# Kernel optimization log

Measured on AMD Instinct MI355X. Metric: run time of the kernel, lower is better.

The kernel has to match this reference:

```python
import jax, jax.numpy as jnp
import numpy as np

HEAD_SIZE = 64


def setup_inputs() -> dict:
    key = jax.random.key(0)
    ks = jax.random.split(key, 6)
    B, S, D, H = 8, 2048, 1024, HEAD_SIZE
    return {
        "q": jax.random.normal(ks[0], (B, S, D), dtype=jnp.float32),
        "k": jax.random.normal(ks[1], (B, S, D), dtype=jnp.float32),
        "v": jax.random.normal(ks[2], (B, S, D), dtype=jnp.float32),
        "mask": jnp.ones((B, S), dtype=bool),
        "Wq": jax.random.normal(ks[3], (D, H), dtype=jnp.float32) * (D ** -0.5),
        "Wk": jax.random.normal(ks[4], (D, H), dtype=jnp.float32) * (D ** -0.5),
        "Wv": jax.random.normal(ks[5], (D, H), dtype=jnp.float32) * (D ** -0.5),
    }


def reference(q, k, v, mask, Wq, Wk, Wv):
    # Linear projections (bias=False): x @ W, W is [n_embd, head_size]
    qp = jnp.einsum("bsd,dh->bsh", q, Wq)
    kp = jnp.einsum("bsd,dh->bsh", k, Wk)
    vp = jnp.einsum("bsd,dh->bsh", v, Wv)
    scale = HEAD_SIZE ** -0.5
    scores = jnp.einsum("bqh,bkh->bqk", qp, kp) * scale  # [B, Sq, Sk]
    # 2-D mask [B, Sk] -> broadcast over query dim (mask.unsqueeze(1))
    scores = jnp.where(mask[:, None, :], scores, -jnp.inf)
    attn = jax.nn.softmax(scores, axis=-1)
    # dropout is identity in eval mode (deterministic reference)
    out = jnp.einsum("bqk,bkh->bqh", attn, vp)
    return out
```

## Files before the change

### kernel.cpp

```cpp
#include <hip/hip_runtime.h>
#include <hip/hip_bf16.h>
#include <math.h>

#define B_ 8
#define S_ 2048
#define D_ 1024
#define H_ 64
#define M_ (B_*S_)
#define SPLIT 4
#define KPS (S_/SPLIT)

typedef __attribute__((ext_vector_type(8))) short bf16x8;
typedef __attribute__((ext_vector_type(8))) unsigned short u16x8;
typedef __attribute__((ext_vector_type(4))) float f32x4;

__device__ inline unsigned short f2bf(float f) {
    unsigned int u = __builtin_bit_cast(unsigned int, f);
    u += 0x7fffu + ((u >> 16) & 1u);
    return (unsigned short)(u >> 16);
}

__device__ inline void async16(const void* g, void* l) {
    __builtin_amdgcn_global_load_lds((const __attribute__((address_space(1))) void*)g,
                                     (__attribute__((address_space(3))) void*)l, 16, 0, 0);
}

__global__ __launch_bounds__(256) void mask_kernel(const unsigned char* __restrict__ mask,
                                                   float* __restrict__ mmul, int n) {
    int j = blockIdx.x * 256 + threadIdx.x;
    if (j >= n) return;
    bool boolLayout = mask[1] != 0;
    int mv = boolLayout ? (int)mask[j] : ((const int*)mask)[j];
    mmul[j] = mv ? 1.0f : 0.0f;
}

__global__ __launch_bounds__(256) void wprep_kernel(
    const float* __restrict__ Wq, const float* __restrict__ Wk, const float* __restrict__ Wv,
    unsigned short* __restrict__ Wt)
{
    const int m = blockIdx.y;
    const float* W = (m == 0) ? Wq : (m == 1) ? Wk : Wv;
    unsigned short* Wo = Wt + (size_t)m * 64 * 1024;
    __shared__ unsigned short T[64][65];
    const int t = threadIdx.x;
    const int k0 = blockIdx.x * 64;
    #pragma unroll
    for (int i = 0; i < 16; i++) {
        int vi = t + i * 256;
        int kk = vi >> 6, n = vi & 63;
        T[kk][n] = f2bf(W[(size_t)(k0 + kk) * 64 + n]);
    }
    __syncthreads();
    #pragma unroll
    for (int i = 0; i < 4; i++) {
        int vi = t + i * 256;
        int n = vi >> 4, k4 = vi & 15;
        ushort4 u;
        u.x = T[k4*4+0][n]; u.y = T[k4*4+1][n]; u.z = T[k4*4+2][n]; u.w = T[k4*4+3][n];
        *(ushort4*)&Wo[(size_t)n * 1024 + k0 + k4*4] = u;
    }
}

__global__ __launch_bounds__(256) void proj_kernel(
    const float* __restrict__ q, const float* __restrict__ kx, const float* __restrict__ vx,
    const unsigned short* __restrict__ Wt,
    unsigned short* __restrict__ qp, unsigned short* __restrict__ kp, unsigned short* __restrict__ vpT)
{
    const int m = blockIdx.y;
    const float* x = (m == 0) ? q : (m == 1) ? kx : vx;
    const unsigned short* Wm = Wt + (size_t)m * 64 * 1024;

    const int t = threadIdx.x;
    const int w = t >> 6, l = t & 63;
    const int lrow = l & 15, quad = l >> 4;
    const int row0 = blockIdx.x * 64;

    const float* xa = x + (size_t)(row0 + w * 16 + lrow) * D_ + quad * 8;
    const unsigned short* wb = Wm + (size_t)lrow * D_ + quad * 8;

    f32x4 acc[4] = {};

    #pragma unroll 2
    for (int k = 0; k < D_; k += 32) {
        f32x4 a0 = *(const f32x4*)(xa + k);
        f32x4 a1 = *(const f32x4*)(xa + k + 4);
        bf16x8 b0 = *(const bf16x8*)(wb + k);
        bf16x8 b1 = *(const bf16x8*)(wb + 16 * D_ + k);
        bf16x8 b2 = *(const bf16x8*)(wb + 32 * D_ + k);
        bf16x8 b3 = *(const bf16x8*)(wb + 48 * D_ + k);
        bf16x8 af;
        af[0] = (short)f2bf(a0.x); af[1] = (short)f2bf(a0.y);
        af[2] = (short)f2bf(a0.z); af[3] = (short)f2bf(a0.w);
        af[4] = (short)f2bf(a1.x); af[5] = (short)f2bf(a1.y);
        af[6] = (short)f2bf(a1.z); af[7] = (short)f2bf(a1.w);
        acc[0] = __builtin_amdgcn_mfma_f32_16x16x32_bf16(af, b0, acc[0], 0, 0, 0);
        acc[1] = __builtin_amdgcn_mfma_f32_16x16x32_bf16(af, b1, acc[1], 0, 0, 0);
        acc[2] = __builtin_amdgcn_mfma_f32_16x16x32_bf16(af, b2, acc[2], 0, 0, 0);
        acc[3] = __builtin_amdgcn_mfma_f32_16x16x32_bf16(af, b3, acc[3], 0, 0, 0);
    }

    const int orow = row0 + w * 16 + quad * 4;
    if (m < 2) {
        unsigned short* outp = (m == 0) ? qp : kp;
        const float sc = (m == 0) ? 0.125f : 1.0f;
        #pragma unroll
        for (int c = 0; c < 4; c++)
            #pragma unroll
            for (int rr = 0; rr < 4; rr++)
                outp[(size_t)(orow + rr) * H_ + c * 16 + lrow] = f2bf(acc[c][rr] * sc);
    } else {
        const int bb = orow >> 11;
        const int s0 = orow & (S_ - 1);
        #pragma unroll
        for (int c = 0; c < 4; c++) {
            ushort4 u;
            u.x = f2bf(acc[c][0]); u.y = f2bf(acc[c][1]);
            u.z = f2bf(acc[c][2]); u.w = f2bf(acc[c][3]);
            *(ushort4*)&vpT[((size_t)bb * H_ + c * 16 + lrow) * S_ + s0] = u;
        }
    }
}

__global__ __launch_bounds__(256) void attn_kernel(
    const unsigned short* __restrict__ qp, const unsigned short* __restrict__ kp,
    const unsigned short* __restrict__ vpT, const float* __restrict__ mmul,
    float* __restrict__ po, float* __restrict__ pl)
{
    __shared__ unsigned short Qs[64][72];
    __shared__ unsigned short Ps[64][72];
    __shared__ unsigned short Ks[64 * 64];
    __shared__ unsigned short Vt[64 * 64];

    const int t = threadIdx.x;
    const int w = t >> 6, l = t & 63;
    const int lrow = l & 15, quad = l >> 4;
    const int b = blockIdx.y, q0 = blockIdx.x * 64, split = blockIdx.z;
    const int key0 = split * KPS;
    const size_t basebs = (size_t)b * S_;
    const unsigned short* vb = vpT + (size_t)b * H_ * S_;

    #pragma unroll
    for (int i = 0; i < 2; i++) {
        int p = t + i * 256;
        int r = p >> 3, c8 = p & 7;
        u16x8 u = *(const u16x8*)&qp[(basebs + q0 + r) * H_ + c8 * 8];
        *(u16x8*)&Qs[r][c8 * 8] = u;
    }

    float lsum[4] = {0.f, 0.f, 0.f, 0.f};
    f32x4 o[4] = {};

    for (int kt = 0; kt < KPS / 64; kt++) {
        const int k0 = key0 + kt * 64;
        __syncthreads();
        #pragma unroll
        for (int j = 0; j < 2; j++) {
            int p = (w * 2 + j) * 64 + l;
            int r = p >> 3;
            int c8 = (p & 7) ^ (r & 7);
            async16(&kp[(basebs + k0 + r) * H_ + c8 * 8], &Ks[p * 8]);
        }
        #pragma unroll
        for (int j = 0; j < 2; j++) {
            int p = (w * 2 + j) * 64 + l;
            int h = p >> 3;
            int c8 = (p & 7) ^ (h & 7);
            async16(&vb[(size_t)h * S_ + k0 + c8 * 8], &Vt[p * 8]);
        }
        float mm[4];
        #pragma unroll
        for (int c = 0; c < 4; c++) mm[c] = mmul[basebs + k0 + c*16 + lrow];
        __syncthreads();

        f32x4 s[4] = {};
        #pragma unroll
        for (int kk = 0; kk < 2; kk++) {
            bf16x8 aq = *(const bf16x8*)&Qs[w*16 + lrow][kk*32 + quad*8];
            #pragma unroll
            for (int c = 0; c < 4; c++) {
                const int n = c*16 + lrow;
                bf16x8 bk = *(const bf16x8*)&Ks[(n * 8 + ((kk*4 + quad) ^ (n & 7))) * 8];
                s[c] = __builtin_amdgcn_mfma_f32_16x16x32_bf16(aq, bk, s[c], 0, 0, 0);
            }
        }
        #pragma unroll
        for (int r = 0; r < 4; r++) {
            float p0 = __expf(s[0][r]) * mm[0];
            float p1 = __expf(s[1][r]) * mm[1];
            float p2 = __expf(s[2][r]) * mm[2];
            float p3 = __expf(s[3][r]) * mm[3];
            lsum[r] += (p0 + p1) + (p2 + p3);
            const int pr = w*16 + quad*4 + r;
            Ps[pr][ 0 + lrow] = f2bf(p0);
            Ps[pr][16 + lrow] = f2bf(p1);
            Ps[pr][32 + lrow] = f2bf(p2);
            Ps[pr][48 + lrow] = f2bf(p3);
        }
        #pragma unroll
        for (int kk = 0; kk < 2; kk++) {
            bf16x8 ap = *(const bf16x8*)&Ps[w*16 + lrow][kk*32 + quad*8];
            #pragma unroll
            for (int c = 0; c < 4; c++) {
                const int h = c*16 + lrow;
                bf16x8 bv = *(const bf16x8*)&Vt[(h * 8 + ((kk*4 + quad) ^ (h & 7))) * 8];
                o[c] = __builtin_amdgcn_mfma_f32_16x16x32_bf16(ap, bv, o[c], 0, 0, 0);
            }
        }
    }

    float* pob = po + (size_t)split * M_ * H_;
    float* plb = pl + (size_t)split * M_;
    #pragma unroll
    for (int r = 0; r < 4; r++) {
        #pragma unroll
        for (int d = 1; d < 16; d <<= 1)
            lsum[r] += __shfl_xor(lsum[r], d, 64);
        const size_t row = basebs + q0 + w*16 + quad*4 + r;
        if (lrow == 0) plb[row] = lsum[r];
        #pragma unroll
        for (int c = 0; c < 4; c++)
            pob[row * H_ + c*16 + lrow] = o[c][r];
    }
}

__global__ __launch_bounds__(256) void combine_kernel(
    const float* __restrict__ po, const float* __restrict__ pl, float* __restrict__ out)
{
    const int idx = blockIdx.x * 256 + threadIdx.x;
    const size_t row = idx >> 4;
    const int c4 = (idx & 15) * 4;
    float lt = 0.f;
    #pragma unroll
    for (int s = 0; s < SPLIT; s++) lt += pl[(size_t)s * M_ + row];
    f32x4 acc = {};
    #pragma unroll
    for (int s = 0; s < SPLIT; s++) {
        const f32x4 p = *(const f32x4*)&po[((size_t)s * M_ + row) * H_ + c4];
        acc += p;
    }
    const float inv = 1.0f / lt;
    f32x4 r = acc * inv;
    *(f32x4*)&out[row * H_ + c4] = r;
}

extern "C" void kernel_launch(void* const* d_in, const int* in_sizes, int n_in,
                              void* d_out, int out_size, void* d_ws, size_t ws_size,
                              hipStream_t stream) {
    const float* q  = (const float*)d_in[0];
    const float* k  = (const float*)d_in[1];
    const float* v  = (const float*)d_in[2];
    const unsigned char* mask = (const unsigned char*)d_in[3];
    const float* Wq = (const float*)d_in[4];
    const float* Wk = (const float*)d_in[5];
    const float* Wv = (const float*)d_in[6];
    float* out = (float*)d_out;

    unsigned short* qp  = (unsigned short*)d_ws;
    unsigned short* kp  = qp + (size_t)M_ * H_;
    unsigned short* vpT = kp + (size_t)M_ * H_;
    float* mmul = (float*)(vpT + (size_t)M_ * H_);
    unsigned short* Wt = (unsigned short*)(mmul + M_);
    float* po = (float*)(Wt + (size_t)3 * 64 * 1024);
    float* pl = po + (size_t)SPLIT * M_ * H_;

    wprep_kernel<<<dim3(16, 3), dim3(256), 0, stream>>>(Wq, Wk, Wv, Wt);
    mask_kernel<<<dim3((M_ + 255)/256), dim3(256), 0, stream>>>(mask, mmul, M_);
    proj_kernel<<<dim3(M_/64, 3), dim3(256), 0, stream>>>(q, k, v, Wt, qp, kp, vpT);
    attn_kernel<<<dim3(S_/64, B_, SPLIT), dim3(256), 0, stream>>>(qp, kp, vpT, mmul, po, pl);
    combine_kernel<<<dim3(M_*16/256), dim3(256), 0, stream>>>(po, pl, out);
}
```

Measured before the change: 250.7 us.

## Stage projection input tiles through LDS with async double-buffered loads

The projection kernel now copies 64x256 fp32 activation tiles into LDS with global_load_lds async copies, using an XOR swizzle and two alternating buffers, so the load of the next K chunk overlaps the MFMA work on the current one. It replaces direct per-lane global loads of the activations. The two buffers take 128 KB of LDS per block, which limits occupancy to about one block per CU. The hand-written vmcnt and barrier sequencing depends on how many loads are in flight.

```diff
diff --git a/kernel.cpp b/kernel.cpp
--- a/kernel.cpp
+++ b/kernel.cpp
@@ -66,6 +66,8 @@
     const unsigned short* __restrict__ Wt,
     unsigned short* __restrict__ qp, unsigned short* __restrict__ kp, unsigned short* __restrict__ vpT)
 {
+    __shared__ float As[2][64 * 256];
+
     const int m = blockIdx.y;
     const float* x = (m == 0) ? q : (m == 1) ? kx : vx;
     const unsigned short* Wm = Wt + (size_t)m * 64 * 1024;
@@ -74,30 +76,57 @@
     const int w = t >> 6, l = t & 63;
     const int lrow = l & 15, quad = l >> 4;
     const int row0 = blockIdx.x * 64;
-
-    const float* xa = x + (size_t)(row0 + w * 16 + lrow) * D_ + quad * 8;
-    const unsigned short* wb = Wm + (size_t)lrow * D_ + quad * 8;
+    const int arow = w * 16 + lrow;
 
     f32x4 acc[4] = {};
 
-    #pragma unroll 2
-    for (int k = 0; k < D_; k += 32) {
-        f32x4 a0 = *(const f32x4*)(xa + k);
-        f32x4 a1 = *(const f32x4*)(xa + k + 4);
-        bf16x8 b0 = *(const bf16x8*)(wb + k);
-        bf16x8 b1 = *(const bf16x8*)(wb + 16 * D_ + k);
-        bf16x8 b2 = *(const bf16x8*)(wb + 32 * D_ + k);
-        bf16x8 b3 = *(const bf16x8*)(wb + 48 * D_ + k);
-        bf16x8 af;
-        af[0] = (short)f2bf(a0.x); af[1] = (short)f2bf(a0.y);
-        af[2] = (short)f2bf(a0.z); af[3] = (short)f2bf(a0.w);
-        af[4] = (short)f2bf(a1.x); af[5] = (short)f2bf(a1.y);
-        af[6] = (short)f2bf(a1.z); af[7] = (short)f2bf(a1.w);
-        acc[0] = __builtin_amdgcn_mfma_f32_16x16x32_bf16(af, b0, acc[0], 0, 0, 0);
-        acc[1] = __builtin_amdgcn_mfma_f32_16x16x32_bf16(af, b1, acc[1], 0, 0, 0);
-        acc[2] = __builtin_amdgcn_mfma_f32_16x16x32_bf16(af, b2, acc[2], 0, 0, 0);
-        acc[3] = __builtin_amdgcn_mfma_f32_16x16x32_bf16(af, b3, acc[3], 0, 0, 0);
-    }
+#define STAGE(s, Ad) do { \
+    _Pragma("unroll") \
+    for (int j_ = 0; j_ < 16; j_++) { \
+        const int row_ = j_ * 4 + w; \
+        async16(x + (size_t)(row0 + row_) * D_ + (s) * 256 + ((l ^ row_) << 2), \
+                (Ad) + row_ * 256 + l * 4); \
+    } \
+    asm volatile("" ::: "memory"); } while (0)
+
+#define COMPUTE(Aa, s) do { \
+    _Pragma("unroll") \
+    for (int kc_ = 0; kc_ < 8; kc_++) { \
+        const int vu_ = kc_ * 8 + quad * 2; \
+        f32x4 a0_ = *(const f32x4*)&(Aa)[arow * 256 + (((vu_    ) ^ arow)) * 4]; \
+        f32x4 a1_ = *(const f32x4*)&(Aa)[arow * 256 + (((vu_ + 1) ^ arow)) * 4]; \
+        bf16x8 af_; \
+        af_[0] = (short)f2bf(a0_.x); af_[1] = (short)f2bf(a0_.y); \
+        af_[2] = (short)f2bf(a0_.z); af_[3] = (short)f2bf(a0_.w); \
+        af_[4] = (short)f2bf(a1_.x); af_[5] = (short)f2bf(a1_.y); \
+        af_[6] = (short)f2bf(a1_.z); af_[7] = (short)f2bf(a1_.w); \
+        _Pragma("unroll") \
+        for (int c_ = 0; c_ < 4; c_++) { \
+            bf16x8 b_ = *(const bf16x8*)&Wm[(size_t)(c_ * 16 + lrow) * 1024 \
+                                            + (s) * 256 + kc_ * 32 + quad * 8]; \
+            acc[c_] = __builtin_amdgcn_mfma_f32_16x16x32_bf16(af_, b_, acc[c_], 0, 0, 0); \
+        } \
+    } } while (0)
+
+#define WAIT16 asm volatile("s_waitcnt vmcnt(16)\n\ts_barrier" ::: "memory")
+#define WAIT0  asm volatile("s_waitcnt vmcnt(0)\n\ts_barrier" ::: "memory")
+#define REUSE_BAR asm volatile("s_barrier" ::: "memory")
+
+    float* A0 = &As[0][0];
+    float* A1 = &As[1][0];
+
+    STAGE(0, A0);
+    STAGE(1, A1);
+    WAIT16; COMPUTE(A0, 0); REUSE_BAR; STAGE(2, A0);
+    WAIT16; COMPUTE(A1, 1); REUSE_BAR; STAGE(3, A1);
+    WAIT16; COMPUTE(A0, 2); REUSE_BAR;
+    WAIT0;  COMPUTE(A1, 3);
+
+#undef STAGE
+#undef COMPUTE
+#undef WAIT16
+#undef WAIT0
+#undef REUSE_BAR
 
     const int orow = row0 + w * 16 + quad * 4;
     if (m < 2) {
```

Result: slower. 274.2 us (+9.4%).
